# Performance work log

Hardware: AMD Instinct MI355X
Metric: run time of the kernel (lower is better)

Reference implementation:

```python
import jax, jax.numpy as jnp
import numpy as np

B, S, V, D, H = 8, 256, 32000, 1024, 1024
NLAY_H, NLAY_L, HEADS = 2, 2, 8
RATIO, N_LOW, N_HIGH = 4, 16, 4
HD = H // HEADS


def setup_inputs():
    key = jax.random.key(0)
    ks = jax.random.split(key, 16)
    s = 0.02
    f = lambda k, shape: (jax.random.normal(k, shape) * s).astype(jnp.float32)
    return {
        "input_ids": jax.random.randint(ks[0], (B, S), 0, V),
        "emb": f(ks[1], (V, D)),
        "pos": f(ks[2], (S, D)),
        "Wih_h": f(ks[3], (NLAY_H, 3 * H, H)),
        "bih_h": jnp.zeros((NLAY_H, 3 * H), jnp.float32),
        "Whh_h": f(ks[4], (NLAY_H, 3 * H, H)),
        "bhh_h": jnp.zeros((NLAY_H, 3 * H), jnp.float32),
        "Win": f(ks[5], (H, 2 * H)),
        "bin_": jnp.zeros((H,), jnp.float32),
        "Wq": f(ks[6], (H, H)),
        "Wk": f(ks[7], (H, H)),
        "Wv": f(ks[8], (H, H)),
        "Wo": f(ks[9], (H, H)),
        "Wih_l": f(ks[10], (NLAY_L, 3 * H, H)),
        "bih_l": jnp.zeros((NLAY_L, 3 * H), jnp.float32),
        "Whh_l": f(ks[11], (NLAY_L, 3 * H, H)),
        "bhh_l": jnp.zeros((NLAY_L, 3 * H), jnp.float32),
        "ln_g": jnp.ones((H,), jnp.float32),
        "ln_b": jnp.zeros((H,), jnp.float32),
        "Wout": f(ks[12], (V, H)),
    }


def gru_cell(x, h, Wih, bih, Whh, bhh):
    gx = x @ Wih.T + bih  # [B, 3H]
    gh = h @ Whh.T + bhh
    xr, xz, xn = jnp.split(gx, 3, axis=-1)
    hr, hz, hn = jnp.split(gh, 3, axis=-1)
    r = jax.nn.sigmoid(xr + hr)
    z = jax.nn.sigmoid(xz + hz)
    n = jnp.tanh(xn + r * hn)
    return (1.0 - z) * n + z * h


def _forward(input_ids, emb, pos, Wih_h, bih_h, Whh_h, bhh_h, Win, bin_,
             Wq, Wk, Wv, Wo, Wih_l, bih_l, Whh_l, bhh_l, ln_g, ln_b, Wout):
    embeds = emb[input_ids] + pos[None, :S]  # [B, S, D]
    inv_sqrt_hd = np.float32(1.0 / np.sqrt(HD))

    def high_mod(x, hs):  # hs: [NLAY_H, B, H]
        new = []
        for l in range(NLAY_H):
            x = gru_cell(x, hs[l], Wih_h[l], bih_h[l], Whh_h[l], bhh_h[l])
            new.append(x)
        return jnp.stack(new), x

    def low_mod(x, high_cur, hist, mask, ls):
        # input projection over [embed ; current high state]
        inp = jax.nn.gelu(jnp.concatenate([x, high_cur], axis=-1) @ Win.T + bin_)  # [B, H]
        # multi-head cross-attention over high-state history (causal in high steps)
        q = (inp @ Wq.T).reshape(B, HEADS, HD)
        k = (hist @ Wk.T).reshape(B, N_HIGH, HEADS, HD)
        v = (hist @ Wv.T).reshape(B, N_HIGH, HEADS, HD)
        scores = jnp.einsum('bhd,bthd->bht', q, k) * inv_sqrt_hd
        scores = jnp.where(mask[None, None, :], scores, jnp.float32(-1e9))
        attn = jax.nn.softmax(scores, axis=-1)
        ctx = jnp.einsum('bht,bthd->bhd', attn, v).reshape(B, H) @ Wo.T
        x2 = inp + ctx
        new = []
        for l in range(NLAY_L):
            x2 = gru_cell(x2, ls[l], Wih_l[l], bih_l[l], Whh_l[l], bhh_l[l])
            new.append(x2)
        return jnp.stack(new), x2

    def step(carry, t):
        hs_all, ls_all, hist = carry
        e = embeds[:, t]  # [B, D]
        low_step = t % N_LOW
        high_step = low_step // RATIO
        do_high = (low_step % RATIO) == 0
        hs = hs_all[high_step]
        new_hs, high_out = high_mod(e, hs)
        hs_all = hs_all.at[high_step].set(jnp.where(do_high, new_hs, hs))
        hist = hist.at[:, high_step].set(jnp.where(do_high, high_out, hist[:, high_step]))
        mask = jnp.arange(N_HIGH) <= high_step
        ls = ls_all[low_step]
        new_ls, low_out = low_mod(e, hist[:, high_step], hist, mask, ls)
        ls_all = ls_all.at[low_step].set(new_ls)
        mu = low_out.mean(axis=-1, keepdims=True)
        var = ((low_out - mu) ** 2).mean(axis=-1, keepdims=True)
        y = (low_out - mu) / jnp.sqrt(var + 1e-5) * ln_g + ln_b
        return (hs_all, ls_all, hist), y @ Wout.T  # [B, V]

    hs0 = jnp.zeros((N_HIGH, NLAY_H, B, H), jnp.float32)
    ls0 = jnp.zeros((N_LOW, NLAY_L, B, H), jnp.float32)
    hist0 = jnp.zeros((B, N_HIGH, H), jnp.float32)
    _, logits = jax.lax.scan(step, (hs0, ls0, hist0), jnp.arange(S))
    return jnp.transpose(logits, (1, 0, 2))  # [B, S, V]


def reference(input_ids, emb, pos, Wih_h, bih_h, Whh_h, bhh_h, Win, bin_,
              Wq, Wk, Wv, Wo, Wih_l, bih_l, Whh_l, bhh_l, ln_g, ln_b, Wout):
    return _forward(input_ids, emb, pos, Wih_h, bih_h, Whh_h, bhh_h, Win, bin_,
                    Wq, Wk, Wv, Wo, Wih_l, bih_l, Whh_l, bhh_l, ln_g, ln_b, Wout)
```

## Files before the change

kernel.cpp:

```cpp
#include <hip/hip_runtime.h>

typedef unsigned short u16;
typedef float f32x4 __attribute__((ext_vector_type(4)));
typedef __bf16 bf16x8 __attribute__((ext_vector_type(8)));
typedef u16 u16x8 __attribute__((ext_vector_type(8)));

#define DEVFN __device__ __forceinline__


DEVFN u16 f2bf(float f) {
  unsigned u = __builtin_bit_cast(unsigned, f);
  unsigned r = u + 0x7FFFu + ((u >> 16) & 1u);
  return (u16)(r >> 16);
}

DEVFN bf16x8 cvt8(const float* p) {
  float4 f0 = *reinterpret_cast<const float4*>(p);
  float4 f1 = *reinterpret_cast<const float4*>(p + 4);
  u16x8 u;
  u[0] = f2bf(f0.x); u[1] = f2bf(f0.y); u[2] = f2bf(f0.z); u[3] = f2bf(f0.w);
  u[4] = f2bf(f1.x); u[5] = f2bf(f1.y); u[6] = f2bf(f1.z); u[7] = f2bf(f1.w);
  return __builtin_bit_cast(bf16x8, u);
}

// ... 181 lines not shown
  gload16(gB + 16 * 1024 + 32, lB1 + BUFO);

  for (int kt = 0; kt < 32; ++kt) {
    int buf = kt % 3;
    __builtin_amdgcn_sched_barrier(0);
    if (kt < 31) asm volatile("s_waitcnt vmcnt(4)" ::: "memory");
    else         asm volatile("s_waitcnt vmcnt(0)" ::: "memory");
    __builtin_amdgcn_s_barrier();
    asm volatile("" ::: "memory");
    if (kt < 30) {
      int k0 = (kt + 2) << 5;
      int bo = ((kt + 2) % 3) * BUFO;
      gload16(gA + k0, lA0 + bo);
      gload16(gA + 16 * 1024 + k0, lA1 + bo);
      gload16(gB + k0, lB0 + bo);
      gload16(gB + 16 * 1024 + k0, lB1 + bo);
    }
    int bb = buf * (BUFO * 2);
    bf16x8 av[4], bv[4];
#pragma unroll
    for (int i = 0; i < 4; ++i) {
      av[i] = *(const bf16x8*)(baseA + bb + offA[i]);
      bv[i] = *(const bf16x8*)(baseB + bb + offB[i]);
    }
#pragma unroll
    for (int mi = 0; mi < 4; ++mi)
#pragma unroll
      for (int ni = 0; ni < 4; ++ni)
        acc[mi][ni] = __builtin_amdgcn_mfma_f32_16x16x32_bf16(av[mi], bv[ni], acc[mi][ni], 0, 0, 0);
  }

  int rb = (lane >> 4) << 2;
#pragma unroll
  for (int mi = 0; mi < 4; ++mi)
#pragma unroll
    for (int ni = 0; ni < 4; ++ni)
#pragma unroll
      for (int rr = 0; rr < 4; ++rr) {
        int row = m0 + qm + mi * 16 + rb + rr;
        int col = n0 + qn + ni * 16 + lr;
        size_t o = (size_t)row * (size_t)ldo + col;
        float v = acc[mi][ni][rr];
        if constexpr (CADD) v += Cadd[o];
        if constexpr (OUTF) {
          if constexpr (NTSTORE) __builtin_nontemporal_store(v, &OUT[o]);
          else OUT[o] = v;
        }
        if constexpr (BF16OUT) OUTbf[o] = f2bf(v);
      }
}

template<int MT, int NT, int KW>
__global__ __launch_bounds__(64 * KW) void gemm2(
    const u16* __restrict__ A, int lda,
    const void* __restrict__ Wp, int ldw, int kwoff, int wbf,
    const float* __restrict__ Cadd, int ldc,
    float* __restrict__ OUT, u16* __restrict__ OUTbf, int ldo, int K) {
  int tid = threadIdx.x;
  int kw = tid >> 6;
  int lane = tid & 63;
  int lr = lane & 15;
  int kk = (lane >> 4) << 3;
  int n0 = blockIdx.x * (16 * NT);
  int m0 = blockIdx.y * (16 * MT);
  int KP = K / KW;
  int kb = kw * KP + kk;

  f32x4 acc[MT][NT];
#pragma unroll
  for (int mi = 0; mi < MT; ++mi)
#pragma unroll
    for (int ni = 0; ni < NT; ++ni) acc[mi][ni] = f32x4{0.f, 0.f, 0.f, 0.f};

  const u16* ap[MT];
#pragma unroll
  for (int mi = 0; mi < MT; ++mi) ap[mi] = A + (size_t)(m0 + mi * 16 + lr) * (size_t)lda + kb;

  if (wbf) {
    const u16* wb[NT];
#pragma unroll
    for (int ni = 0; ni < NT; ++ni)
      wb[ni] = (const u16*)Wp + (size_t)(n0 + ni * 16 + lr) * (size_t)ldw + kwoff + kb;
    for (int k0 = 0; k0 < KP; k0 += 32) {
      bf16x8 wv[NT];
#pragma unroll
      for (int ni = 0; ni < NT; ++ni) wv[ni] = ldbf(wb[ni] + k0);
#pragma unroll
      for (int mi = 0; mi < MT; ++mi) {
        bf16x8 a = ldbf(ap[mi] + k0);
#pragma unroll
        for (int ni = 0; ni < NT; ++ni)
          acc[mi][ni] = __builtin_amdgcn_mfma_f32_16x16x32_bf16(a, wv[ni], acc[mi][ni], 0, 0, 0);
      }
    }
  } else {
    const float* wf[NT];
#pragma unroll
    for (int ni = 0; ni < NT; ++ni)
      wf[ni] = (const float*)Wp + (size_t)(n0 + ni * 16 + lr) * (size_t)ldw + kwoff + kb;
    for (int k0 = 0; k0 < KP; k0 += 32) {
      bf16x8 wv[NT];
#pragma unroll
      for (int ni = 0; ni < NT; ++ni) wv[ni] = cvt8(wf[ni] + k0);
#pragma unroll
      for (int mi = 0; mi < MT; ++mi) {
        bf16x8 a = ldbf(ap[mi] + k0);
#pragma unroll
        for (int ni = 0; ni < NT; ++ni)
          acc[mi][ni] = __builtin_amdgcn_mfma_f32_16x16x32_bf16(a, wv[ni], acc[mi][ni], 0, 0, 0);
      }
    }
  }

  if constexpr (KW > 1) {
    __shared__ f32x4 red[KW][MT * NT][64];
#pragma unroll
    for (int mi = 0; mi < MT; ++mi)
#pragma unroll
      for (int ni = 0; ni < NT; ++ni) red[kw][mi * NT + ni][lane] = acc[mi][ni];
    __syncthreads();
    if (kw) return;
    for (int w2 = 1; w2 < KW; ++w2)
#pragma unroll
      for (int mi = 0; mi < MT; ++mi)
#pragma unroll
        for (int ni = 0; ni < NT; ++ni) acc[mi][ni] += red[w2][mi * NT + ni][lane];
  }

  int rb = (lane >> 4) << 2;
#pragma unroll
  for (int mi = 0; mi < MT; ++mi)
#pragma unroll
    for (int ni = 0; ni < NT; ++ni)
#pragma unroll
      for (int rr = 0; rr < 4; ++rr) {
        int row = m0 + mi * 16 + rb + rr;
        int col = n0 + ni * 16 + lr;
        size_t o = (size_t)row * (size_t)ldo + col;
        float v = acc[mi][ni][rr];
        if (Cadd) v += Cadd[(size_t)row * (size_t)ldc + col];
        if (OUT) OUT[o] = v;
        if (OUTbf) OUTbf[o] = f2bf(v);
      }
}

DEVFN void gru_step_body(const u16* __restrict__ X, const u16* __restrict__ Hb,
                         const float* __restrict__ Hf,
                         const u16* __restrict__ Wih, const u16* __restrict__ Whh,
                         const float* __restrict__ bih, const float* __restrict__ bhh,
                         const float* __restrict__ gx,
                         float* __restrict__ Hof, u16* __restrict__ Hob,
                         u16* __restrict__ hist,
                         int m0, int j0, int kw, int lane,
                         f32x4 (*red)[8][64]) {
  int lr = lane & 15;
  int kk = (lane >> 4) << 3;
  const int KP = 256;
  int kb = kw * KP + kk;

  f32x4 aR[2], aZ[2], aNX[2], aNH[2];
#pragma unroll
  for (int mi = 0; mi < 2; ++mi) {
    aR[mi] = f32x4{0.f, 0.f, 0.f, 0.f};
    aZ[mi] = f32x4{0.f, 0.f, 0.f, 0.f};
    aNX[mi] = f32x4{0.f, 0.f, 0.f, 0.f};
    aNH[mi] = f32x4{0.f, 0.f, 0.f, 0.f};
  }

  const u16* hp[2];
#pragma unroll
  for (int mi = 0; mi < 2; ++mi)
    hp[mi] = Hb + (size_t)(m0 + mi * 16 + lr) * 1024 + kb;

  size_t wro = (size_t)(j0 + lr) * 1024 + kb;
  const u16 *phr = Whh + wro, *phz = Whh + wro + 1048576, *phn = Whh + wro + 2097152;

  if (gx) {
    for (int k0 = 0; k0 < KP; k0 += 32) {
      bf16x8 whr = ldbf(phr + k0), whz = ldbf(phz + k0), whn = ldbf(phn + k0);
#pragma unroll
      for (int mi = 0; mi < 2; ++mi) {
        bf16x8 ah = ldbf(hp[mi] + k0);
        aR[mi] = __builtin_amdgcn_mfma_f32_16x16x32_bf16(ah, whr, aR[mi], 0, 0, 0);
        aZ[mi] = __builtin_amdgcn_mfma_f32_16x16x32_bf16(ah, whz, aZ[mi], 0, 0, 0);
        aNH[mi] = __builtin_amdgcn_mfma_f32_16x16x32_bf16(ah, whn, aNH[mi], 0, 0, 0);
      }
    }
  } else {
    const u16* xp[2];
#pragma unroll
    for (int mi = 0; mi < 2; ++mi)
      xp[mi] = X + (size_t)(m0 + mi * 16 + lr) * 1024 + kb;
    const u16 *pxr = Wih + wro, *pxz = Wih + wro + 1048576, *pxn = Wih + wro + 2097152;
    for (int k0 = 0; k0 < KP; k0 += 32) {
      bf16x8 wxr = ldbf(pxr + k0), wxz = ldbf(pxz + k0), wxn = ldbf(pxn + k0);
      bf16x8 whr = ldbf(phr + k0), whz = ldbf(phz + k0), whn = ldbf(phn + k0);
#pragma unroll
      for (int mi = 0; mi < 2; ++mi) {
        bf16x8 ax = ldbf(xp[mi] + k0);
        bf16x8 ah = ldbf(hp[mi] + k0);
        aR[mi] = __builtin_amdgcn_mfma_f32_16x16x32_bf16(ax, wxr, aR[mi], 0, 0, 0);
        aR[mi] = __builtin_amdgcn_mfma_f32_16x16x32_bf16(ah, whr, aR[mi], 0, 0, 0);
        aZ[mi] = __builtin_amdgcn_mfma_f32_16x16x32_bf16(ax, wxz, aZ[mi], 0, 0, 0);
        aZ[mi] = __builtin_amdgcn_mfma_f32_16x16x32_bf16(ah, whz, aZ[mi], 0, 0, 0);
        aNX[mi] = __builtin_amdgcn_mfma_f32_16x16x32_bf16(ax, wxn, aNX[mi], 0, 0, 0);
        aNH[mi] = __builtin_amdgcn_mfma_f32_16x16x32_bf16(ah, whn, aNH[mi], 0, 0, 0);
      }
    }
  }

#pragma unroll
  for (int mi = 0; mi < 2; ++mi) {
    red[kw][mi * 4 + 0][lane] = aR[mi];
    red[kw][mi * 4 + 1][lane] = aZ[mi];
    red[kw][mi * 4 + 2][lane] = aNX[mi];
    red[kw][mi * 4 + 3][lane] = aNH[mi];
  }
  __syncthreads();
  if (kw == 0) {
    for (int w2 = 1; w2 < 4; ++w2)
#pragma unroll
      for (int mi = 0; mi < 2; ++mi) {
        aR[mi] += red[w2][mi * 4 + 0][lane];
        aZ[mi] += red[w2][mi * 4 + 1][lane];
        aNX[mi] += red[w2][mi * 4 + 2][lane];
        aNH[mi] += red[w2][mi * 4 + 3][lane];
      }
    int c = j0 + lr;
    float br = bih[c] + bhh[c];
    float bz = bih[1024 + c] + bhh[1024 + c];
    float bnx = bih[2048 + c];
    float bnh = bhh[2048 + c];
    int rb = (lane >> 4) << 2;
#pragma unroll
    for (int mi = 0; mi < 2; ++mi)
#pragma unroll
      for (int rr = 0; rr < 4; ++rr) {
        int row = m0 + mi * 16 + rb + rr;
        float gr = 0.f, gz = 0.f, gn = 0.f;
        if (gx) {
          const float* gp = gx + (size_t)row * 3072;
          gr = gp[c]; gz = gp[1024 + c]; gn = gp[2048 + c];
        }
        float r = sigm(gr + aR[mi][rr] + br);
        float z = sigm(gz + aZ[mi][rr] + bz);
        float n = tanhf(gn + aNX[mi][rr] + bnx + r * (aNH[mi][rr] + bnh));
        size_t o = (size_t)row * 1024 + c;
        float hv = (1.f - z) * n + z * Hf[o];
        Hof[o] = hv;
        u16 hb = f2bf(hv);
        Hob[o] = hb;
        if (hist) hist[o] = hb;
      }
  }
}

struct GruP {
  const u16* X; const u16* Hb; const float* Hf;
  const u16* Wbih; const u16* Wbhh;
  const float* Wfih; const float* Wfhh;
  const float* bih; const float* bhh;
  const float* gx;
  float* Hof; u16* Hob; u16* hist;
};
struct FoldSeg { const float* src; u16* dst; };
struct FoldArgs { FoldSeg s[7]; long long pref[8]; long long base; long long total; int nseg; };

__global__ __launch_bounds__(256) void gru_dual(GruP pa, GruP pb, int tiles1,
                                                int tiles_total, int wbf, FoldArgs fa) {
  int yy = (int)blockIdx.y;
  if (yy >= tiles_total) {
    if (fa.total == 0) return;
    long long L = (long long)(yy - tiles_total) * gridDim.x + blockIdx.x;
    long long off = fa.base + L * 2048;
    if (off >= fa.total) return;
    int s = 0;
    while (off >= fa.pref[s + 1]) ++s;
    long long local = off - fa.pref[s] + ((long long)threadIdx.x << 3);
    *reinterpret_cast<u16x8*>(fa.s[s].dst + local) =
        __builtin_bit_cast(u16x8, cvt8(fa.s[s].src + local));
    return;
  }

  GruP p; int m0;
  if (yy < tiles1) { p = pa; m0 = yy * 32; }
  else { p = pb; m0 = (yy - tiles1) * 32; }
  int tid = threadIdx.x;
  int kw = tid >> 6;
  int lane = tid & 63;
  __shared__ f32x4 red[4][8][64];
  int j0 = blockIdx.x * 16;

  if (wbf) {
    gru_step_body(p.X, p.Hb, p.Hf, p.Wbih, p.Wbhh, p.bih, p.bhh, p.gx,
                  p.Hof, p.Hob, p.hist, m0, j0, kw, lane, red);
    return;
  }

  int lr = lane & 15;
  int kk = (lane >> 4) << 3;
  const int KP = 256;
  int kb = kw * KP + kk;
  f32x4 aR[2], aZ[2], aNX[2], aNH[2];
#pragma unroll
  for (int mi = 0; mi < 2; ++mi) {
    aR[mi] = f32x4{0.f, 0.f, 0.f, 0.f};
    aZ[mi] = f32x4{0.f, 0.f, 0.f, 0.f};
    aNX[mi] = f32x4{0.f, 0.f, 0.f, 0.f};
    aNH[mi] = f32x4{0.f, 0.f, 0.f, 0.f};
  }
  const u16* xp[2];
  const u16* hp[2];
#pragma unroll
  for (int mi = 0; mi < 2; ++mi) {
    size_t ro = (size_t)(m0 + mi * 16 + lr) * 1024 + kb;
    xp[mi] = p.X + ro;
    hp[mi] = p.Hb + ro;
  }
  size_t wro = (size_t)(j0 + lr) * 1024 + kb;
  const float *pxr = p.Wfih + wro, *pxz = p.Wfih + wro + 1048576, *pxn = p.Wfih + wro + 2097152;
  const float *phr = p.Wfhh + wro, *phz = p.Wfhh + wro + 1048576, *phn = p.Wfhh + wro + 2097152;
  for (int k0 = 0; k0 < KP; k0 += 32) {
    bf16x8 wxr = cvt8(pxr + k0), wxz = cvt8(pxz + k0), wxn = cvt8(pxn + k0);
    bf16x8 whr = cvt8(phr + k0), whz = cvt8(phz + k0), whn = cvt8(phn + k0);
#pragma unroll
    for (int mi = 0; mi < 2; ++mi) {
      bf16x8 ax = ldbf(xp[mi] + k0);
      bf16x8 ah = ldbf(hp[mi] + k0);
      aR[mi] = __builtin_amdgcn_mfma_f32_16x16x32_bf16(ax, wxr, aR[mi], 0, 0, 0);
      aR[mi] = __builtin_amdgcn_mfma_f32_16x16x32_bf16(ah, whr, aR[mi], 0, 0, 0);
      aZ[mi] = __builtin_amdgcn_mfma_f32_16x16x32_bf16(ax, wxz, aZ[mi], 0, 0, 0);
      aZ[mi] = __builtin_amdgcn_mfma_f32_16x16x32_bf16(ah, whz, aZ[mi], 0, 0, 0);
      aNX[mi] = __builtin_amdgcn_mfma_f32_16x16x32_bf16(ax, wxn, aNX[mi], 0, 0, 0);
      aNH[mi] = __builtin_amdgcn_mfma_f32_16x16x32_bf16(ah, whn, aNH[mi], 0, 0, 0);
    }
  }
#pragma unroll
  for (int mi = 0; mi < 2; ++mi) {
    red[kw][mi * 4 + 0][lane] = aR[mi];
    red[kw][mi * 4 + 1][lane] = aZ[mi];
    red[kw][mi * 4 + 2][lane] = aNX[mi];
    red[kw][mi * 4 + 3][lane] = aNH[mi];
  }
  __syncthreads();
  if (kw) return;
  for (int w2 = 1; w2 < 4; ++w2)
#pragma unroll
    for (int mi = 0; mi < 2; ++mi) {
      aR[mi] += red[w2][mi * 4 + 0][lane];
      aZ[mi] += red[w2][mi * 4 + 1][lane];
      aNX[mi] += red[w2][mi * 4 + 2][lane];
      aNH[mi] += red[w2][mi * 4 + 3][lane];
    }
  int c = j0 + lr;
  float br = p.bih[c] + p.bhh[c];
  float bz = p.bih[1024 + c] + p.bhh[1024 + c];
  float bnx = p.bih[2048 + c];
  float bnh = p.bhh[2048 + c];
  int rb = (lane >> 4) << 2;
#pragma unroll
  for (int mi = 0; mi < 2; ++mi)
#pragma unroll
    for (int rr = 0; rr < 4; ++rr) {
      int row = m0 + mi * 16 + rb + rr;
      float r = sigm(aR[mi][rr] + br);
      float z = sigm(aZ[mi][rr] + bz);
      float n = tanhf(aNX[mi][rr] + bnx + r * (aNH[mi][rr] + bnh));
      size_t o = (size_t)row * 1024 + c;
      float hv = (1.f - z) * n + z * p.Hf[o];
      p.Hof[o] = hv;
      u16 hb = f2bf(hv);
      p.Hob[o] = hb;
      if (p.hist) p.hist[o] = hb;
    }
}

__global__ __launch_bounds__(256) void gemm_big(const u16* __restrict__ A,
                                                const void* __restrict__ Wp, int wbf,
                                                float* __restrict__ OUT) {
  int wv = threadIdx.x >> 6;
  int lane = threadIdx.x & 63;
  int lr = lane & 15;
  int kk = (lane >> 4) << 3;
  int m0 = blockIdx.x * 256 + wv * 64;
  int n0 = blockIdx.y * 64;

  f32x4 acc[4][4];
#pragma unroll
  for (int mi = 0; mi < 4; ++mi)
#pragma unroll
    for (int ni = 0; ni < 4; ++ni) acc[mi][ni] = f32x4{0.f, 0.f, 0.f, 0.f};

  const u16* ap[4];
#pragma unroll
  for (int mi = 0; mi < 4; ++mi) ap[mi] = A + (size_t)(m0 + mi * 16 + lr) * 1024 + kk;

  const float* wf[4];
#pragma unroll
  for (int ni = 0; ni < 4; ++ni) wf[ni] = (const float*)Wp + (size_t)(n0 + ni * 16 + lr) * 1024 + kk;
  for (int k0 = 0; k0 < 1024; k0 += 32) {
    bf16x8 wvv[4];
#pragma unroll
    for (int ni = 0; ni < 4; ++ni) wvv[ni] = cvt8(wf[ni] + k0);
#pragma unroll
    for (int mi = 0; mi < 4; ++mi) {
      bf16x8 a = ldbf(ap[mi] + k0);
#pragma unroll
      for (int ni = 0; ni < 4; ++ni)
        acc[mi][ni] = __builtin_amdgcn_mfma_f32_16x16x32_bf16(a, wvv[ni], acc[mi][ni], 0, 0, 0);
    }
  }

  int rb = (lane >> 4) << 2;
#pragma unroll
  for (int mi = 0; mi < 4; ++mi)
#pragma unroll
    for (int ni = 0; ni < 4; ++ni)
#pragma unroll
      for (int rr = 0; rr < 4; ++rr) {
        size_t o = (size_t)(m0 + mi * 16 + rb + rr) * 32000 + (size_t)(n0 + ni * 16 + lr);
        __builtin_nontemporal_store(acc[mi][ni][rr], &OUT[o]);
      }
}

struct CvtSeg { const float* src; u16* dst; int src_ld; int col_off; int log2c; int nblk; };
struct CvtArgs { CvtSeg seg[11]; int nseg; };

__global__ void cvt_all(CvtArgs a) {
  int blk = blockIdx.x;
  int s = 0;
  while (s < a.nseg - 1 && blk >= a.seg[s].nblk) { blk -= a.seg[s].nblk; ++s; }
  const CvtSeg g = a.seg[s];
  size_t idx = ((size_t)blk * 256 + threadIdx.x) * 8;
  size_t row = idx >> g.log2c;
  int col = (int)(idx & ((1u << g.log2c) - 1));
  const float* sp = g.src + row * (size_t)g.src_ld + g.col_off + col;
  *reinterpret_cast<u16x8*>(g.dst + idx) = __builtin_bit_cast(u16x8, cvt8(sp));
}

__global__ void embed_kernel(const int* __restrict__ ids, const float* __restrict__ emb,
                             const float* __restrict__ pos, u16* __restrict__ out,
                             u16* __restrict__ hiX) {
  int idx = blockIdx.x * 256 + threadIdx.x;
  int e8 = (idx & 127) << 3;
  int rb = idx >> 7;
  int t = rb >> 3, b = rb & 7;
  int w = t >> 4, lsp = t & 15, g = lsp >> 2, o = lsp & 3;
  int R = ((w << 4) + (o << 2) + g) * 8 + b;
  int tok = ids[b * 256 + t];
  const float* ep = emb + (size_t)tok * 1024 + e8;
  const float* pp = pos + (size_t)t * 1024 + e8;
  u16x8 u;
#pragma unroll
  for (int i = 0; i < 8; ++i) u[i] = f2bf(ep[i] + pp[i]);
  *reinterpret_cast<u16x8*>(out + (size_t)R * 1024 + e8) = u;
  if (o == 0)
    *reinterpret_cast<u16x8*>(hiX + (size_t)(w * 32 + g * 8 + b) * 1024 + e8) = u;
}

__global__ void inp_all(const float* __restrict__ einp, const float* __restrict__ kvhAll,
                        const float* __restrict__ bin, float* __restrict__ inpb,
                        u16* __restrict__ inpbf) {
  int idx = blockIdx.x * 256 + threadIdx.x;
  int r = idx >> 10, j = idx & 1023;
  int w = r >> 7, r7 = r & 127;
  int g = (r7 >> 3) & 3, b = r7 & 7;
  float x = einp[idx] + kvhAll[(size_t)(w * 32 + g * 8 + b) * 3072 + 2048 + j] + bin[j];
  float t = tanhf(0.7978845608028654f * (x + 0.044715f * x * x * x));
  float v = 0.5f * x * (1.f + t);
  inpb[idx] = v;
  inpbf[idx] = f2bf(v);
}

__global__ void attn_all(const float* __restrict__ qb, const float* __restrict__ kvhAll,
                         u16* __restrict__ ctxbf) {
  int r = blockIdx.x;
  int w = r >> 7, r7 = r & 127;
  int sp = r7 >> 3;
  int g = sp & 3;
  int b = r7 & 7;
  int lane = threadIdx.x;
  const float* kvb = kvhAll + (size_t)w * 32 * 3072;
  __shared__ float aw[8][4];
  if (lane < 32) {
    int head = lane >> 2, t = lane & 3;
    float s = 0.f;
    if (t <= g) {
      const float* qp = qb + (size_t)r * 1024 + head * 128;
      const float* kp = kvb + (size_t)(t * 8 + b) * 3072 + head * 128;
      for (int d = 0; d < 128; ++d) s += qp[d] * kp[d];
      s *= 0.08838834764831845f;
    }
    float sc[4];
    sc[0] = __shfl(s, (head << 2) + 0);
    sc[1] = __shfl(s, (head << 2) + 1);
    sc[2] = __shfl(s, (head << 2) + 2);
    sc[3] = __shfl(s, (head << 2) + 3);
    if (t == 0) {
      float mx = -1e30f;
      for (int u = 0; u <= g; ++u) mx = fmaxf(mx, sc[u]);
      float p[4] = {0.f, 0.f, 0.f, 0.f};
      float den = 0.f;
      for (int u = 0; u <= g; ++u) { p[u] = expf(sc[u] - mx); den += p[u]; }
      float inv = 1.f / den;
      for (int u = 0; u < 4; ++u) aw[head][u] = (u <= g) ? p[u] * inv : 0.f;
    }
  }
  __syncthreads();
  for (int idx = lane; idx < 1024; idx += 64) {
    int head = idx >> 7;
    float acc = 0.f;
#pragma unroll
    for (int t = 0; t < 4; ++t) acc += aw[head][t] * kvb[(size_t)(t * 8 + b) * 3072 + 1024 + idx];
    ctxbf[(size_t)r * 1024 + idx] = f2bf(acc);
  }
}

__global__ void ln_all(const float* __restrict__ ls1f, const float* __restrict__ g_,
                       const float* __restrict__ b_, u16* __restrict__ Ybf) {
  int bid = blockIdx.x;
  int w = bid >> 7, r7 = bid & 127;
  int tid = threadIdx.x;
  const float* x = ls1f + (size_t)(w + 1) * 131072 + (size_t)r7 * 1024;
  float s = 0.f, s2 = 0.f;
  for (int j = tid; j < 1024; j += 256) { float v = x[j]; s += v; s2 += v * v; }
  for (int off = 32; off; off >>= 1) { s += __shfl_xor(s, off); s2 += __shfl_xor(s2, off); }
  __shared__ float rs[4], rs2[4], mv[2];
  int wv = tid >> 6;
  if ((tid & 63) == 0) { rs[wv] = s; rs2[wv] = s2; }
  __syncthreads();
  if (tid == 0) {
    float S = rs[0] + rs[1] + rs[2] + rs[3];
    float S2 = rs2[0] + rs2[1] + rs2[2] + rs2[3];
    float mu = S * (1.f / 1024.f);
    float var = S2 * (1.f / 1024.f) - mu * mu;
    mv[0] = mu;
    mv[1] = rsqrtf(var + 1e-5f);
  }
  __syncthreads();
  float mu = mv[0], rstd = mv[1];
  int sp = r7 >> 3, b = r7 & 7;
  int g = sp & 3, o = sp >> 2;
  int t = w * 16 + g * 4 + o;
  u16* yrow = Ybf + (size_t)(b * 256 + t) * 1024;
  for (int j = tid; j < 1024; j += 256) {
    float v = (x[j] - mu) * rstd * g_[j] + b_[j];
    yrow[j] = f2bf(v);
  }
}

extern "C" void kernel_launch(void* const* d_in, const int* in_sizes, int n_in,
                              void* d_out, int out_size, void* d_ws, size_t ws_size,
                              hipStream_t stream) {
  const int* ids = (const int*)d_in[0];
  const float* emb = (const float*)d_in[1];
  const float* pos = (const float*)d_in[2];
  const float* Wih_h = (const float*)d_in[3];
  const float* bih_h = (const float*)d_in[4];
  const float* Whh_h = (const float*)d_in[5];
  const float* bhh_h = (const float*)d_in[6];
  const float* Win = (const float*)d_in[7];
  const float* bin_ = (const float*)d_in[8];
  const float* Wq = (const float*)d_in[9];
  const float* Wk = (const float*)d_in[10];
  const float* Wv = (const float*)d_in[11];
  const float* Wo = (const float*)d_in[12];
  const float* Wih_l = (const float*)d_in[13];
  const float* bih_l = (const float*)d_in[14];
  const float* Whh_l = (const float*)d_in[15];
  const float* bhh_l = (const float*)d_in[16];
  const float* ln_g = (const float*)d_in[17];
  const float* ln_b = (const float*)d_in[18];
  const float* Wout = (const float*)d_in[19];
  float* out = (float*)d_out;

  size_t off = 0;
  char* wsb = (char*)d_ws;
  auto allocF = [&](size_t n) { float* p = (float*)(wsb + off); off += n * 4; return p; };
  auto allocU = [&](size_t n) { u16* p = (u16*)(wsb + off); off += n * 2; return p; };

  float* hs0f = allocF((size_t)17 * 32768);
  float* hs1f = allocF((size_t)17 * 32768);
  float* ls0f = allocF((size_t)17 * 131072);
  float* ls1f = allocF((size_t)17 * 131072);
  u16* hs0b = allocU((size_t)17 * 32768);
  u16* hs1b = allocU((size_t)17 * 32768);
  u16* ls0b = allocU((size_t)17 * 131072);
  u16* ls1b = allocU((size_t)17 * 131072);
  u16* histAll = allocU(524288);
  u16* embB = allocU(2097152);
  u16* hiX = allocU(524288);
  float* einp = allocF(2097152);
  float* kvhAll = allocF((size_t)512 * 3072);
  float* inpb = allocF(2097152);
  u16* inpbf = allocU(2097152);
  float* qb = allocF(2097152);
  u16* ctxbf = allocU(2097152);
  u16* x2bf = allocU(2097152);
  u16* Ybf = allocU(2097152);
  float* GXH = allocF((size_t)512 * 3072);
  float* GXL = allocF((size_t)2048 * 3072);

  const size_t WPACK_BYTES = (size_t)(4 * 6291456 + 1048576 + 1048576 + 1048576 + 3145728) * 2;
  bool packW = (off + WPACK_BYTES <= ws_size);
  u16 *WihHb = nullptr, *WhhHb = nullptr, *WihLb = nullptr, *WhhLb = nullptr;
  u16 *WinB0 = nullptr, *WqB = nullptr, *WoB = nullptr, *KVp = nullptr;
  if (packW) {
    WihHb = allocU(6291456);
    WhhHb = allocU(6291456);
    WihLb = allocU(6291456);
    WhhLb = allocU(6291456);
    WinB0 = allocU(1048576);
    WqB = allocU(1048576);
    WoB = allocU(1048576);
    KVp = allocU(3145728);
  }
  bool packWout = packW && (off + (size_t)32768000 * 2 <= ws_size);
  u16* WoutB = nullptr;
  if (packWout) WoutB = allocU(32768000);

  (void)hipMemsetAsync(hs0f, 0, 32768 * 4, stream);
  (void)hipMemsetAsync(hs1f, 0, 32768 * 4, stream);
  (void)hipMemsetAsync(ls0f, 0, 131072 * 4, stream);
  (void)hipMemsetAsync(ls1f, 0, 131072 * 4, stream);
  (void)hipMemsetAsync(hs0b, 0, 32768 * 2, stream);
  (void)hipMemsetAsync(hs1b, 0, 32768 * 2, stream);
  (void)hipMemsetAsync(ls0b, 0, 131072 * 2, stream);
  (void)hipMemsetAsync(ls1b, 0, 131072 * 2, stream);

  embed_kernel<<<1024, 256, 0, stream>>>(ids, emb, pos, embB, hiX);
  if (packW) {
    CvtArgs ca{};
    int ns = 0, tot = 0;
    auto add = [&](const float* s, u16* d, int ld, int co, int l2c, size_t nelem) {
      int nb = (int)(nelem / 2048);
      ca.seg[ns++] = CvtSeg{s, d, ld, co, l2c, nb};
      tot += nb;
    };
    add(Wih_h, WihHb, 1024, 0, 10, 6291456);
    add(Whh_h, WhhHb, 1024, 0, 10, 6291456);
    add(Win, WinB0, 2048, 0, 10, 1048576);
    add(Win, KVp + 2097152, 2048, 1024, 10, 1048576);
    ca.nseg = ns;
    cvt_all<<<tot, 256, 0, stream>>>(ca);
  }
  int wbfW = packW ? 1 : 0;

  FoldArgs fa{};
  fa.total = 0;
  FoldArgs fz{};
  fz.total = 0;
  long long bpd = 0;
  int extraY = 0;
  if (packW) {
    int ns = 0;
    long long pref = 0;
    auto addF = [&](const float* s, u16* d, long long n) {
      fa.s[ns].src = s; fa.s[ns].dst = d; fa.pref[ns] = pref; pref += n; ++ns;
    };
    addF(Wih_l, WihLb, 6291456);
    addF(Whh_l, WhhLb, 6291456);
    addF(Wq, WqB, 1048576);
    addF(Wo, WoB, 1048576);
    addF(Wk, KVp, 1048576);
    addF(Wv, KVp + 1048576, 1048576);
    if (packWout) addF(Wout, WoutB, 32768000);
    fa.pref[ns] = pref;
    fa.total = pref;
    fa.nseg = ns;
    long long tb = pref / 2048;
    bpd = (tb + 16) / 17;
    extraY = (int)((bpd + 63) / 64);
  }

  if (packW) {
    gemm_lds<0, 1, 0, 0><<<128, 256, 0, stream>>>(embB, WinB0, nullptr, einp, nullptr, 1024, 16);
    gemm_lds<0, 1, 0, 0><<<96, 256, 0, stream>>>(hiX, WihHb, nullptr, GXH, nullptr, 3072, 4);
  } else {
    gemm2<2, 2, 2><<<dim3(32, 64), 128, 0, stream>>>(
        embB, 1024, Win, 2048, 0, 0, nullptr, 0, einp, nullptr, 1024, 1024);
  }

  const size_t LW = (size_t)3072 * 1024;
  auto HP = [&](int layer, int w) {
    GruP p;
    if (layer == 0) {
      p.X = embB + (size_t)w * 131072;
      p.Hb = hs0b + (size_t)w * 32768; p.Hf = hs0f + (size_t)w * 32768;
      p.Wbih = WihHb; p.Wbhh = WhhHb; p.Wfih = Wih_h; p.Wfhh = Whh_h;
      p.bih = bih_h; p.bhh = bhh_h;
      p.gx = packW ? (GXH + (size_t)w * 32 * 3072) : nullptr;
      p.Hof = hs0f + (size_t)(w + 1) * 32768; p.Hob = hs0b + (size_t)(w + 1) * 32768;
      p.hist = nullptr;
    } else {
      p.X = hs0b + (size_t)(w + 1) * 32768;
      p.Hb = hs1b + (size_t)w * 32768; p.Hf = hs1f + (size_t)w * 32768;
      p.Wbih = WihHb ? WihHb + LW : nullptr; p.Wbhh = WhhHb ? WhhHb + LW : nullptr;
      p.Wfih = Wih_h + LW; p.Wfhh = Whh_h + LW;
      p.bih = bih_h + 3072; p.bhh = bhh_h + 3072;
      p.gx = nullptr;
      p.Hof = hs1f + (size_t)(w + 1) * 32768; p.Hob = hs1b + (size_t)(w + 1) * 32768;
      p.hist = histAll + (size_t)w * 32768;
    }
    return p;
  };
  auto LP = [&](int layer, int w) {
    GruP p;
    if (layer == 0) {
      p.X = x2bf + (size_t)w * 131072;
      p.Hb = ls0b + (size_t)w * 131072; p.Hf = ls0f + (size_t)w * 131072;
      p.Wbih = WihLb; p.Wbhh = WhhLb; p.Wfih = Wih_l; p.Wfhh = Whh_l;
      p.bih = bih_l; p.bhh = bhh_l;
      p.gx = packW ? (GXL + (size_t)w * 128 * 3072) : nullptr;
      p.Hof = ls0f + (size_t)(w + 1) * 131072; p.Hob = ls0b + (size_t)(w + 1) * 131072;
      p.hist = nullptr;
    } else {
      p.X = ls0b + (size_t)(w + 1) * 131072;
      p.Hb = ls1b + (size_t)w * 131072; p.Hf = ls1f + (size_t)w * 131072;
      p.Wbih = WihLb ? WihLb + LW : nullptr; p.Wbhh = WhhLb ? WhhLb + LW : nullptr;
      p.Wfih = Wih_l + LW; p.Wfhh = Whh_l + LW;
      p.bih = bih_l + 3072; p.bhh = bhh_l + 3072;
      p.gx = nullptr;
      p.Hof = ls1f + (size_t)(w + 1) * 131072; p.Hob = ls1b + (size_t)(w + 1) * 131072;
      p.hist = nullptr;
    }
    return p;
  };

  auto launch_high = [&](GruP pa, GruP pb, int t1, int ttot, int d) {
    if (packW && fa.total) {
      fa.base = (long long)d * bpd * 2048;
      gru_dual<<<dim3(64, ttot + extraY), 256, 0, stream>>>(pa, pb, t1, ttot, wbfW, fa);
    } else {
      gru_dual<<<dim3(64, ttot), 256, 0, stream>>>(pa, pb, t1, ttot, wbfW, fz);
    }
  };
  launch_high(HP(0, 0), HP(0, 0), 1, 1, 0);
  for (int d = 1; d <= 15; ++d) launch_high(HP(1, d - 1), HP(0, d), 1, 2, d);
  launch_high(HP(1, 15), HP(1, 15), 1, 1, 16);

  if (packW) {
    gemm_lds<0, 1, 0, 0><<<96, 256, 0, stream>>>(histAll, KVp, nullptr, kvhAll, nullptr, 3072, 4);
  } else {
    gemm2<2, 2, 2><<<dim3(32, 16), 128, 0, stream>>>(
        histAll, 1024, Wk, 1024, 0, 0, nullptr, 0, kvhAll, nullptr, 3072, 1024);
    gemm2<2, 2, 2><<<dim3(32, 16), 128, 0, stream>>>(
        histAll, 1024, Wv, 1024, 0, 0, nullptr, 0, kvhAll + 1024, nullptr, 3072, 1024);
    gemm2<2, 2, 2><<<dim3(32, 16), 128, 0, stream>>>(
        histAll, 1024, Win, 2048, 1024, 0, nullptr, 0, kvhAll + 2048, nullptr, 3072, 1024);
  }
  inp_all<<<8192, 256, 0, stream>>>(einp, kvhAll, bin_, inpb, inpbf);
  if (packW)
    gemm_lds<0, 1, 0, 0><<<128, 256, 0, stream>>>(inpbf, WqB, nullptr, qb, nullptr, 1024, 16);
  else
    gemm2<2, 2, 2><<<dim3(32, 64), 128, 0, stream>>>(
        inpbf, 1024, Wq, 1024, 0, 0, nullptr, 0, qb, nullptr, 1024, 1024);
  attn_all<<<2048, 64, 0, stream>>>(qb, kvhAll, ctxbf);
  if (packW) {
    gemm_lds<0, 0, 1, 1><<<128, 256, 0, stream>>>(ctxbf, WoB, inpb, nullptr, x2bf, 1024, 16);
    gemm_lds<0, 1, 0, 0><<<384, 256, 0, stream>>>(x2bf, WihLb, nullptr, GXL, nullptr, 3072, 16);
  } else {
    gemm2<2, 2, 2><<<dim3(32, 64), 128, 0, stream>>>(
        ctxbf, 1024, Wo, 1024, 0, 0, inpb, 1024, nullptr, x2bf, 1024, 1024);
  }

  gru_dual<<<dim3(64, 4), 256, 0, stream>>>(LP(0, 0), LP(0, 0), 4, 4, wbfW, fz);
  for (int d = 1; d <= 15; ++d)
    gru_dual<<<dim3(64, 8), 256, 0, stream>>>(LP(1, d - 1), LP(0, d), 4, 8, wbfW, fz);
  gru_dual<<<dim3(64, 4), 256, 0, stream>>>(LP(1, 15), LP(1, 15), 4, 4, wbfW, fz);

  ln_all<<<2048, 256, 0, stream>>>(ls1f, ln_g, ln_b, Ybf);
  if (packWout)
    gemm8<<<1000, 512, 0, stream>>>(Ybf, WoutB, out);
  else
    gemm_big<<<dim3(8, 500), 256, 0, stream>>>(Ybf, Wout, 0, out);
}
```

Measured before the change: 1.045 ms.

## Halve GRU row tiles and double K-split waves for more parallelism

The GRU step kernel now computes 16-row tiles instead of 32 and splits K across 8 waves (512 threads) instead of 4. Launch grids are doubled in y and the weight-fold chunk per block is doubled to match. This puts more blocks and waves on the latency-bound recurrent steps. The cost is that weights are re-read by twice as many row tiles and the shared-memory reduction has more partials. Separately, eight hipMemsetAsync calls are replaced by one fused zeroing kernel to cut launch overhead.

```diff
diff --git a/kernel.cpp b/kernel.cpp
--- a/kernel.cpp
+++ b/kernel.cpp
@@ -357,106 +357,84 @@
                          float* __restrict__ Hof, u16* __restrict__ Hob,
                          u16* __restrict__ hist,
                          int m0, int j0, int kw, int lane,
-                         f32x4 (*red)[8][64]) {
+                         f32x4 (*red)[4][64]) {
   int lr = lane & 15;
   int kk = (lane >> 4) << 3;
-  const int KP = 256;
+  const int KP = 128;
   int kb = kw * KP + kk;
 
-  f32x4 aR[2], aZ[2], aNX[2], aNH[2];
-#pragma unroll
-  for (int mi = 0; mi < 2; ++mi) {
-    aR[mi] = f32x4{0.f, 0.f, 0.f, 0.f};
-    aZ[mi] = f32x4{0.f, 0.f, 0.f, 0.f};
-    aNX[mi] = f32x4{0.f, 0.f, 0.f, 0.f};
-    aNH[mi] = f32x4{0.f, 0.f, 0.f, 0.f};
-  }
-
-  const u16* hp[2];
-#pragma unroll
-  for (int mi = 0; mi < 2; ++mi)
-    hp[mi] = Hb + (size_t)(m0 + mi * 16 + lr) * 1024 + kb;
-
+  f32x4 aR = f32x4{0.f, 0.f, 0.f, 0.f};
+  f32x4 aZ = f32x4{0.f, 0.f, 0.f, 0.f};
+  f32x4 aNX = f32x4{0.f, 0.f, 0.f, 0.f};
+  f32x4 aNH = f32x4{0.f, 0.f, 0.f, 0.f};
+
+  const u16* hp = Hb + (size_t)(m0 + lr) * 1024 + kb;
   size_t wro = (size_t)(j0 + lr) * 1024 + kb;
   const u16 *phr = Whh + wro, *phz = Whh + wro + 1048576, *phn = Whh + wro + 2097152;
 
   if (gx) {
+#pragma unroll
     for (int k0 = 0; k0 < KP; k0 += 32) {
       bf16x8 whr = ldbf(phr + k0), whz = ldbf(phz + k0), whn = ldbf(phn + k0);
-#pragma unroll
-      for (int mi = 0; mi < 2; ++mi) {
-        bf16x8 ah = ldbf(hp[mi] + k0);
-        aR[mi] = __builtin_amdgcn_mfma_f32_16x16x32_bf16(ah, whr, aR[mi], 0, 0, 0);
-        aZ[mi] = __builtin_amdgcn_mfma_f32_16x16x32_bf16(ah, whz, aZ[mi], 0, 0, 0);
-        aNH[mi] = __builtin_amdgcn_mfma_f32_16x16x32_bf16(ah, whn, aNH[mi], 0, 0, 0);
-      }
+      bf16x8 ah = ldbf(hp + k0);
+      aR = __builtin_amdgcn_mfma_f32_16x16x32_bf16(ah, whr, aR, 0, 0, 0);
+      aZ = __builtin_amdgcn_mfma_f32_16x16x32_bf16(ah, whz, aZ, 0, 0, 0);
+      aNH = __builtin_amdgcn_mfma_f32_16x16x32_bf16(ah, whn, aNH, 0, 0, 0);
     }
   } else {
-    const u16* xp[2];
-#pragma unroll
-    for (int mi = 0; mi < 2; ++mi)
-      xp[mi] = X + (size_t)(m0 + mi * 16 + lr) * 1024 + kb;
+    const u16* xp = X + (size_t)(m0 + lr) * 1024 + kb;
     const u16 *pxr = Wih + wro, *pxz = Wih + wro + 1048576, *pxn = Wih + wro + 2097152;
+#pragma unroll
     for (int k0 = 0; k0 < KP; k0 += 32) {
       bf16x8 wxr = ldbf(pxr + k0), wxz = ldbf(pxz + k0), wxn = ldbf(pxn + k0);
       bf16x8 whr = ldbf(phr + k0), whz = ldbf(phz + k0), whn = ldbf(phn + k0);
-#pragma unroll
-      for (int mi = 0; mi < 2; ++mi) {
-        bf16x8 ax = ldbf(xp[mi] + k0);
-        bf16x8 ah = ldbf(hp[mi] + k0);
-        aR[mi] = __builtin_amdgcn_mfma_f32_16x16x32_bf16(ax, wxr, aR[mi], 0, 0, 0);
-        aR[mi] = __builtin_amdgcn_mfma_f32_16x16x32_bf16(ah, whr, aR[mi], 0, 0, 0);
-        aZ[mi] = __builtin_amdgcn_mfma_f32_16x16x32_bf16(ax, wxz, aZ[mi], 0, 0, 0);
-        aZ[mi] = __builtin_amdgcn_mfma_f32_16x16x32_bf16(ah, whz, aZ[mi], 0, 0, 0);
-        aNX[mi] = __builtin_amdgcn_mfma_f32_16x16x32_bf16(ax, wxn, aNX[mi], 0, 0, 0);
-        aNH[mi] = __builtin_amdgcn_mfma_f32_16x16x32_bf16(ah, whn, aNH[mi], 0, 0, 0);
-      }
-    }
-  }
-
-#pragma unroll
-  for (int mi = 0; mi < 2; ++mi) {
-    red[kw][mi * 4 + 0][lane] = aR[mi];
-    red[kw][mi * 4 + 1][lane] = aZ[mi];
-    red[kw][mi * 4 + 2][lane] = aNX[mi];
-    red[kw][mi * 4 + 3][lane] = aNH[mi];
-  }
+      bf16x8 ax = ldbf(xp + k0);
+      bf16x8 ah = ldbf(hp + k0);
+      aR = __builtin_amdgcn_mfma_f32_16x16x32_bf16(ax, wxr, aR, 0, 0, 0);
+      aR = __builtin_amdgcn_mfma_f32_16x16x32_bf16(ah, whr, aR, 0, 0, 0);
+      aZ = __builtin_amdgcn_mfma_f32_16x16x32_bf16(ax, wxz, aZ, 0, 0, 0);
+      aZ = __builtin_amdgcn_mfma_f32_16x16x32_bf16(ah, whz, aZ, 0, 0, 0);
+      aNX = __builtin_amdgcn_mfma_f32_16x16x32_bf16(ax, wxn, aNX, 0, 0, 0);
+      aNH = __builtin_amdgcn_mfma_f32_16x16x32_bf16(ah, whn, aNH, 0, 0, 0);
+    }
+  }
+
+  red[kw][0][lane] = aR;
+  red[kw][1][lane] = aZ;
+  red[kw][2][lane] = aNX;
+  red[kw][3][lane] = aNH;
   __syncthreads();
   if (kw == 0) {
-    for (int w2 = 1; w2 < 4; ++w2)
-#pragma unroll
-      for (int mi = 0; mi < 2; ++mi) {
-        aR[mi] += red[w2][mi * 4 + 0][lane];
-        aZ[mi] += red[w2][mi * 4 + 1][lane];
-        aNX[mi] += red[w2][mi * 4 + 2][lane];
-        aNH[mi] += red[w2][mi * 4 + 3][lane];
-      }
+    for (int w2 = 1; w2 < 8; ++w2) {
+      aR += red[w2][0][lane];
+      aZ += red[w2][1][lane];
+      aNX += red[w2][2][lane];
+      aNH += red[w2][3][lane];
+    }
     int c = j0 + lr;
     float br = bih[c] + bhh[c];
     float bz = bih[1024 + c] + bhh[1024 + c];
     float bnx = bih[2048 + c];
     float bnh = bhh[2048 + c];
-    int rb = (lane >> 4) << 2;
-#pragma unroll
-    for (int mi = 0; mi < 2; ++mi)
-#pragma unroll
-      for (int rr = 0; rr < 4; ++rr) {
-        int row = m0 + mi * 16 + rb + rr;
-        float gr = 0.f, gz = 0.f, gn = 0.f;
-        if (gx) {
-          const float* gp = gx + (size_t)row * 3072;
-          gr = gp[c]; gz = gp[1024 + c]; gn = gp[2048 + c];
-        }
-        float r = sigm(gr + aR[mi][rr] + br);
-        float z = sigm(gz + aZ[mi][rr] + bz);
-        float n = tanhf(gn + aNX[mi][rr] + bnx + r * (aNH[mi][rr] + bnh));
-        size_t o = (size_t)row * 1024 + c;
-        float hv = (1.f - z) * n + z * Hf[o];
-        Hof[o] = hv;
-        u16 hb = f2bf(hv);
-        Hob[o] = hb;
-        if (hist) hist[o] = hb;
+    int rb2 = (lane >> 4) << 2;
+#pragma unroll
+    for (int rr = 0; rr < 4; ++rr) {
+      int row = m0 + rb2 + rr;
+      float gr = 0.f, gz = 0.f, gn = 0.f;
+      if (gx) {
+        const float* gp = gx + (size_t)row * 3072;
+        gr = gp[c]; gz = gp[1024 + c]; gn = gp[2048 + c];
       }
+      float r = sigm(gr + aR[rr] + br);
+      float z = sigm(gz + aZ[rr] + bz);
+      float n = tanhf(gn + aNX[rr] + bnx + r * (aNH[rr] + bnh));
+      size_t o = (size_t)row * 1024 + c;
+      float hv = (1.f - z) * n + z * Hf[o];
+      Hof[o] = hv;
+      u16 hb = f2bf(hv);
+      Hob[o] = hb;
+      if (hist) hist[o] = hb;
+    }
   }
 }
 
@@ -471,13 +449,13 @@
 struct FoldSeg { const float* src; u16* dst; };
 struct FoldArgs { FoldSeg s[7]; long long pref[8]; long long base; long long total; int nseg; };
 
-__global__ __launch_bounds__(256) void gru_dual(GruP pa, GruP pb, int tiles1,
+__global__ __launch_bounds__(512) void gru_dual(GruP pa, GruP pb, int tiles1,
                                                 int tiles_total, int wbf, FoldArgs fa) {
   int yy = (int)blockIdx.y;
   if (yy >= tiles_total) {
     if (fa.total == 0) return;
     long long L = (long long)(yy - tiles_total) * gridDim.x + blockIdx.x;
-    long long off = fa.base + L * 2048;
+    long long off = fa.base + L * 4096;
     if (off >= fa.total) return;
     int s = 0;
     while (off >= fa.pref[s + 1]) ++s;
@@ -488,12 +466,12 @@
   }
 
   GruP p; int m0;
-  if (yy < tiles1) { p = pa; m0 = yy * 32; }
-  else { p = pb; m0 = (yy - tiles1) * 32; }
+  if (yy < tiles1) { p = pa; m0 = yy * 16; }
+  else { p = pb; m0 = (yy - tiles1) * 16; }
   int tid = threadIdx.x;
   int kw = tid >> 6;
   int lane = tid & 63;
-  __shared__ f32x4 red[4][8][64];
+  __shared__ f32x4 red[8][4][64];
   int j0 = blockIdx.x * 16;
 
   if (wbf) {
@@ -504,80 +482,60 @@
 
   int lr = lane & 15;
   int kk = (lane >> 4) << 3;
-  const int KP = 256;
+  const int KP = 128;
   int kb = kw * KP + kk;
-  f32x4 aR[2], aZ[2], aNX[2], aNH[2];
-#pragma unroll
-  for (int mi = 0; mi < 2; ++mi) {
-    aR[mi] = f32x4{0.f, 0.f, 0.f, 0.f};
-    aZ[mi] = f32x4{0.f, 0.f, 0.f, 0.f};
-    aNX[mi] = f32x4{0.f, 0.f, 0.f, 0.f};
-    aNH[mi] = f32x4{0.f, 0.f, 0.f, 0.f};
-  }
-  const u16* xp[2];
-  const u16* hp[2];
-#pragma unroll
-  for (int mi = 0; mi < 2; ++mi) {
-    size_t ro = (size_t)(m0 + mi * 16 + lr) * 1024 + kb;
-    xp[mi] = p.X + ro;
-    hp[mi] = p.Hb + ro;
-  }
+  f32x4 aR = f32x4{0.f, 0.f, 0.f, 0.f};
+  f32x4 aZ = f32x4{0.f, 0.f, 0.f, 0.f};
+  f32x4 aNX = f32x4{0.f, 0.f, 0.f, 0.f};
+  f32x4 aNH = f32x4{0.f, 0.f, 0.f, 0.f};
+  const u16* xp = p.X + (size_t)(m0 + lr) * 1024 + kb;
+  const u16* hp = p.Hb + (size_t)(m0 + lr) * 1024 + kb;
   size_t wro = (size_t)(j0 + lr) * 1024 + kb;
   const float *pxr = p.Wfih + wro, *pxz = p.Wfih + wro + 1048576, *pxn = p.Wfih + wro + 2097152;
   const float *phr = p.Wfhh + wro, *phz = p.Wfhh + wro + 1048576, *phn = p.Wfhh + wro + 2097152;
   for (int k0 = 0; k0 < KP; k0 += 32) {
     bf16x8 wxr = cvt8(pxr + k0), wxz = cvt8(pxz + k0), wxn = cvt8(pxn + k0);
     bf16x8 whr = cvt8(phr + k0), whz = cvt8(phz + k0), whn = cvt8(phn + k0);
-#pragma unroll
-    for (int mi = 0; mi < 2; ++mi) {
-      bf16x8 ax = ldbf(xp[mi] + k0);
-      bf16x8 ah = ldbf(hp[mi] + k0);
-      aR[mi] = __builtin_amdgcn_mfma_f32_16x16x32_bf16(ax, wxr, aR[mi], 0, 0, 0);
-      aR[mi] = __builtin_amdgcn_mfma_f32_16x16x32_bf16(ah, whr, aR[mi], 0, 0, 0);
-      aZ[mi] = __builtin_amdgcn_mfma_f32_16x16x32_bf16(ax, wxz, aZ[mi], 0, 0, 0);
-      aZ[mi] = __builtin_amdgcn_mfma_f32_16x16x32_bf16(ah, whz, aZ[mi], 0, 0, 0);
-      aNX[mi] = __builtin_amdgcn_mfma_f32_16x16x32_bf16(ax, wxn, aNX[mi], 0, 0, 0);
-      aNH[mi] = __builtin_amdgcn_mfma_f32_16x16x32_bf16(ah, whn, aNH[mi], 0, 0, 0);
-    }
-  }
-#pragma unroll
-  for (int mi = 0; mi < 2; ++mi) {
-    red[kw][mi * 4 + 0][lane] = aR[mi];
-    red[kw][mi * 4 + 1][lane] = aZ[mi];
-    red[kw][mi * 4 + 2][lane] = aNX[mi];
-    red[kw][mi * 4 + 3][lane] = aNH[mi];
-  }
+    bf16x8 ax = ldbf(xp + k0);
+    bf16x8 ah = ldbf(hp + k0);
+    aR = __builtin_amdgcn_mfma_f32_16x16x32_bf16(ax, wxr, aR, 0, 0, 0);
+    aR = __builtin_amdgcn_mfma_f32_16x16x32_bf16(ah, whr, aR, 0, 0, 0);
+    aZ = __builtin_amdgcn_mfma_f32_16x16x32_bf16(ax, wxz, aZ, 0, 0, 0);
+    aZ = __builtin_amdgcn_mfma_f32_16x16x32_bf16(ah, whz, aZ, 0, 0, 0);
+    aNX = __builtin_amdgcn_mfma_f32_16x16x32_bf16(ax, wxn, aNX, 0, 0, 0);
+    aNH = __builtin_amdgcn_mfma_f32_16x16x32_bf16(ah, whn, aNH, 0, 0, 0);
+  }
+  red[kw][0][lane] = aR;
+  red[kw][1][lane] = aZ;
+  red[kw][2][lane] = aNX;
+  red[kw][3][lane] = aNH;
   __syncthreads();
   if (kw) return;
-  for (int w2 = 1; w2 < 4; ++w2)
-#pragma unroll
-    for (int mi = 0; mi < 2; ++mi) {
-      aR[mi] += red[w2][mi * 4 + 0][lane];
-      aZ[mi] += red[w2][mi * 4 + 1][lane];
-      aNX[mi] += red[w2][mi * 4 + 2][lane];
-      aNH[mi] += red[w2][mi * 4 + 3][lane];
-    }
+  for (int w2 = 1; w2 < 8; ++w2) {
+    aR += red[w2][0][lane];
+    aZ += red[w2][1][lane];
+    aNX += red[w2][2][lane];
+    aNH += red[w2][3][lane];
+  }
   int c = j0 + lr;
   float br = p.bih[c] + p.bhh[c];
   float bz = p.bih[1024 + c] + p.bhh[1024 + c];
   float bnx = p.bih[2048 + c];
   float bnh = p.bhh[2048 + c];
-  int rb = (lane >> 4) << 2;
-#pragma unroll
-  for (int mi = 0; mi < 2; ++mi)
-#pragma unroll
-    for (int rr = 0; rr < 4; ++rr) {
-      int row = m0 + mi * 16 + rb + rr;
-      float r = sigm(aR[mi][rr] + br);
-      float z = sigm(aZ[mi][rr] + bz);
-      float n = tanhf(aNX[mi][rr] + bnx + r * (aNH[mi][rr] + bnh));
-      size_t o = (size_t)row * 1024 + c;
-      float hv = (1.f - z) * n + z * p.Hf[o];
-      p.Hof[o] = hv;
-      u16 hb = f2bf(hv);
-      p.Hob[o] = hb;
-      if (p.hist) p.hist[o] = hb;
-    }
+  int rb2 = (lane >> 4) << 2;
+#pragma unroll
+  for (int rr = 0; rr < 4; ++rr) {
+    int row = m0 + rb2 + rr;
+    float r = sigm(aR[rr] + br);
+    float z = sigm(aZ[rr] + bz);
+    float n = tanhf(aNX[rr] + bnx + r * (aNH[rr] + bnh));
+    size_t o = (size_t)row * 1024 + c;
+    float hv = (1.f - z) * n + z * p.Hf[o];
+    p.Hof[o] = hv;
+    u16 hb = f2bf(hv);
+    p.Hob[o] = hb;
+    if (p.hist) p.hist[o] = hb;
+  }
 }
 
 __global__ __launch_bounds__(256) void gemm_big(const u16* __restrict__ A,
@@ -641,6 +599,15 @@
   int col = (int)(idx & ((1u << g.log2c) - 1));
   const float* sp = g.src + row * (size_t)g.src_ld + g.col_off + col;
   *reinterpret_cast<u16x8*>(g.dst + idx) = __builtin_bit_cast(u16x8, cvt8(sp));
+}
+
+struct ZeroArgs { unsigned* p[8]; long long pref[9]; };
+__global__ void zero8(ZeroArgs z) {
+  long long i = (long long)blockIdx.x * 256 + threadIdx.x;
+  if (i >= z.pref[8]) return;
+  int s = 0;
+  while (i >= z.pref[s + 1]) ++s;
+  z.p[s][i - z.pref[s]] = 0u;
 }
 
 __global__ void embed_kernel(const int* __restrict__ ids, const float* __restrict__ emb,
@@ -824,14 +791,18 @@
   u16* WoutB = nullptr;
   if (packWout) WoutB = allocU(32768000);
 
-  (void)hipMemsetAsync(hs0f, 0, 32768 * 4, stream);
-  (void)hipMemsetAsync(hs1f, 0, 32768 * 4, stream);
-  (void)hipMemsetAsync(ls0f, 0, 131072 * 4, stream);
-  (void)hipMemsetAsync(ls1f, 0, 131072 * 4, stream);
-  (void)hipMemsetAsync(hs0b, 0, 32768 * 2, stream);
-  (void)hipMemsetAsync(hs1b, 0, 32768 * 2, stream);
-  (void)hipMemsetAsync(ls0b, 0, 131072 * 2, stream);
-  (void)hipMemsetAsync(ls1b, 0, 131072 * 2, stream);
+  {
+    ZeroArgs z;
+    long long pf = 0;
+    int si = 0;
+    auto addZ = [&](void* p, long long words) {
+      z.p[si] = (unsigned*)p; z.pref[si] = pf; pf += words; ++si;
+    };
+    addZ(hs0f, 32768); addZ(hs1f, 32768); addZ(ls0f, 131072); addZ(ls1f, 131072);
+    addZ(hs0b, 16384); addZ(hs1b, 16384); addZ(ls0b, 65536); addZ(ls1b, 65536);
+    z.pref[8] = pf;
+    zero8<<<(int)((pf + 255) / 256), 256, 0, stream>>>(z);
+  }
 
   embed_kernel<<<1024, 256, 0, stream>>>(ids, emb, pos, embB, hiX);
   if (packW) {
@@ -873,7 +844,7 @@
     fa.pref[ns] = pref;
     fa.total = pref;
     fa.nseg = ns;
-    long long tb = pref / 2048;
+    long long tb = pref / 4096;
     bpd = (tb + 16) / 17;
     extraY = (int)((bpd + 63) / 64);
   }
@@ -934,15 +905,15 @@
 
   auto launch_high = [&](GruP pa, GruP pb, int t1, int ttot, int d) {
     if (packW && fa.total) {
-      fa.base = (long long)d * bpd * 2048;
-      gru_dual<<<dim3(64, ttot + extraY), 256, 0, stream>>>(pa, pb, t1, ttot, wbfW, fa);
+      fa.base = (long long)d * bpd * 4096;
+      gru_dual<<<dim3(64, ttot + extraY), 512, 0, stream>>>(pa, pb, t1, ttot, wbfW, fa);
     } else {
-      gru_dual<<<dim3(64, ttot), 256, 0, stream>>>(pa, pb, t1, ttot, wbfW, fz);
+      gru_dual<<<dim3(64, ttot), 512, 0, stream>>>(pa, pb, t1, ttot, wbfW, fz);
     }
   };
-  launch_high(HP(0, 0), HP(0, 0), 1, 1, 0);
-  for (int d = 1; d <= 15; ++d) launch_high(HP(1, d - 1), HP(0, d), 1, 2, d);
-  launch_high(HP(1, 15), HP(1, 15), 1, 1, 16);
+  launch_high(HP(0, 0), HP(0, 0), 2, 2, 0);
+  for (int d = 1; d <= 15; ++d) launch_high(HP(1, d - 1), HP(0, d), 2, 4, d);
+  launch_high(HP(1, 15), HP(1, 15), 2, 2, 16);
 
   if (packW) {
     gemm_lds<0, 1, 0, 0><<<96, 256, 0, stream>>>(histAll, KVp, nullptr, kvhAll, nullptr, 3072, 4);
@@ -969,10 +940,10 @@
         ctxbf, 1024, Wo, 1024, 0, 0, inpb, 1024, nullptr, x2bf, 1024, 1024);
   }
 
-  gru_dual<<<dim3(64, 4), 256, 0, stream>>>(LP(0, 0), LP(0, 0), 4, 4, wbfW, fz);
+  gru_dual<<<dim3(64, 8), 512, 0, stream>>>(LP(0, 0), LP(0, 0), 8, 8, wbfW, fz);
   for (int d = 1; d <= 15; ++d)
-    gru_dual<<<dim3(64, 8), 256, 0, stream>>>(LP(1, d - 1), LP(0, d), 4, 8, wbfW, fz);
-  gru_dual<<<dim3(64, 4), 256, 0, stream>>>(LP(1, 15), LP(1, 15), 4, 4, wbfW, fz);
+    gru_dual<<<dim3(64, 16), 512, 0, stream>>>(LP(1, d - 1), LP(0, d), 8, 16, wbfW, fz);
+  gru_dual<<<dim3(64, 8), 512, 0, stream>>>(LP(1, 15), LP(1, 15), 8, 8, wbfW, fz);
 
   ln_all<<<2048, 256, 0, stream>>>(ls1f, ln_g, ln_b, Ybf);
   if (packWout)
```

After: 1.082 ms. 3.6% more time.
